# Kernel optimization log

Measured on AMD Instinct MI355X. Metric: run time of the kernel, lower is better.

Reference implementation:

```python
import jax, jax.numpy as jnp
import numpy as np

B, L, D, MAXW = 8, 512, 768, 12
H = D // 2  # forward/backward half of the bidirectional encoder output


def setup_inputs() -> dict:
    key = jax.random.key(0)
    k1, k2, k3, k4 = jax.random.split(key, 4)
    h = jax.random.normal(k1, (B, L, D), jnp.float32)
    # ATG-style span enumeration: start=i, end=min(i+w, L-1) for w in [0, MAXW)
    starts = jnp.broadcast_to(jnp.arange(L)[:, None], (L, MAXW))
    ends = jnp.minimum(starts + jnp.arange(MAXW)[None, :], L - 1)
    span_idx = jnp.stack([starts, ends], axis=-1).reshape(1, L * MAXW, 2)
    span_idx = jnp.broadcast_to(span_idx, (B, L * MAXW, 2)).astype(jnp.int64)
    # downproject: Linear(D -> D) since BidirectionalEndpointSpanExtractor output dim == D
    W = jax.random.normal(k2, (D, D), jnp.float32) / np.sqrt(D)
    b = jnp.zeros((D,), jnp.float32)
    # learned sentinels (use_sentinels=True default), one per half
    start_sentinel = jax.random.normal(k3, (H,), jnp.float32) * 0.02
    end_sentinel = jax.random.normal(k4, (H,), jnp.float32) * 0.02
    return {"h": h, "span_idx": span_idx, "W": W, "b": b,
            "start_sentinel": start_sentinel, "end_sentinel": end_sentinel}


def _gather(seq, idx):
    # seq: (B, L, H), idx: (B, S) -> (B, S, H)
    return jnp.take_along_axis(seq, idx[..., None], axis=1)


def reference(h, span_idx, W, b, start_sentinel, end_sentinel):
    Bv, Lv, Dv = h.shape
    Hv = Dv // 2
    fwd, bwd = h[..., :Hv], h[..., Hv:]
    starts = span_idx[..., 0]
    ends = span_idx[..., 1]
    # exclusive endpoints
    excl_starts = starts - 1
    start_mask = excl_starts == -1                 # before sequence start -> start sentinel
    excl_ends = ends + 1
    end_mask = excl_ends >= Lv                     # past sequence end -> end sentinel
    excl_starts = jnp.where(start_mask, 0, excl_starts)
    excl_ends = jnp.where(end_mask, 0, excl_ends)
    f_start = _gather(fwd, excl_starts)            # (B, S, H)
    f_end = _gather(fwd, ends)
    b_start = _gather(bwd, excl_ends)
    b_end = _gather(bwd, starts)
    f_start = jnp.where(start_mask[..., None], start_sentinel, f_start)
    b_start = jnp.where(end_mask[..., None], end_sentinel, b_start)
    # forward_combination='y-x', backward_combination='x-y'
    span_rep = jnp.concatenate([f_end - f_start, b_start - b_end], axis=-1)  # (B, S, D)
    out = jax.nn.relu(jnp.einsum('bsd,ed->bse', span_rep, W) + b)
    return out.reshape(Bv, Lv, -1, Dv)            # (B, L, MAXW, D)
```

## Files before the change

### kernel.cpp

```cpp
#include <hip/hip_runtime.h>

typedef __attribute__((ext_vector_type(4))) float f32x4;
typedef __attribute__((ext_vector_type(8))) _Float16 f16x8;
typedef __attribute__((ext_vector_type(4))) unsigned short u16x4;

#define NB 8
#define LLEN 512
#define DD 768
#define MW 12
#define HH 384
#define TT (NB * LLEN)
#define SS (LLEN * MW)
#define MM (2 * TT)

#define BT 32
#define BE 192
#define WROWS 48
#define PADW 204

#define PACKH_BLOCKS ((TT * 192) / 256)
#define PACKW_BLOCKS ((DD * 192) / 256)
#define SENT_BLOCKS (DD / 4)
#define PREP_BLOCKS (PACKH_BLOCKS + PACKW_BLOCKS + SENT_BLOCKS)

__device__ __forceinline__ unsigned short f2h(float x) {
  _Float16 h = (_Float16)x;
  return __builtin_bit_cast(unsigned short, h);
}
__device__ __forceinline__ float h2f(unsigned short u) {
  return (float)__builtin_bit_cast(_Float16, u);
}
__device__ __forceinline__ void gload_lds16(const void* g, void* l) {
  __builtin_amdgcn_global_load_lds(
      (const __attribute__((address_space(1))) unsigned int*)g,
      (__attribute__((address_space(3))) unsigned int*)l, 16, 0, 0);
}

__global__ __launch_bounds__(256) void prep_k(const float* __restrict__ h,
                                              const float* __restrict__ W,
                                              const float* __restrict__ ss,
                                              const float* __restrict__ es,
                                              unsigned short* __restrict__ A,
                                              unsigned short* __restrict__ Bu,
                                              unsigned short* __restrict__ Bv,
                                              unsigned short* __restrict__ us,
                                              unsigned short* __restrict__ vs) {
  int bid = blockIdx.x;
  if (bid < PACKH_BLOCKS) {
    int idx = bid * 256 + threadIdx.x;
    int t = idx / 192;
    int k = (idx - t * 192) * 4;
    f32x4 f = *(const f32x4*)(h + (size_t)idx * 4);
    int row = (k < HH) ? t : TT + t;
    int kk = (k < HH) ? k : k - HH;
    u16x4 v;
#pragma unroll
    for (int j = 0; j < 4; ++j) v[j] = f2h(f[j]);
    *(u16x4*)(A + (size_t)row * HH + kk) = v;
  } else if (bid < PACKH_BLOCKS + PACKW_BLOCKS) {
    int idx = (bid - PACKH_BLOCKS) * 256 + threadIdx.x;
    int e = idx / 192;
    int k = (idx - e * 192) * 4;
    f32x4 f = *(const f32x4*)(W + (size_t)idx * 4);
    unsigned short* Bm = (k < HH) ? Bu : Bv;
    int kk = (k < HH) ? k : k - HH;
    u16x4 v;
#pragma unroll
    for (int j = 0; j < 4; ++j) v[j] = f2h(f[j]);
    *(u16x4*)(Bm + (size_t)e * HH + kk) = v;
  } else {
    int e = (bid - PACKH_BLOCKS - PACKW_BLOCKS) * 4 + (threadIdx.x >> 6);
    int lane = threadIdx.x & 63;
    float a = 0.f, b = 0.f;
    const float* w = W + (size_t)e * DD;
    for (int j = lane; j < HH; j += 64) {
      a += ss[j] * w[j];
      b += es[j] * w[HH + j];
    }
#pragma unroll
    for (int off = 32; off > 0; off >>= 1) {
      a += __shfl_down(a, off);
      b += __shfl_down(b, off);
    }
    if (lane == 0) { us[e] = f2h(a); vs[e] = f2h(b); }
  }
}

__global__ __launch_bounds__(256) void fused_k(const unsigned short* __restrict__ A,
                                               const unsigned short* __restrict__ Bu,
                                               const unsigned short* __restrict__ Bv,
                                               const int* __restrict__ span,
                                               const unsigned short* __restrict__ us,
                                               const unsigned short* __restrict__ vs,
                                               const float* __restrict__ bias,
                                               float* __restrict__ out) {
  __shared__ char lds[96 * 64 * 2 + 2 * 192 * 64 * 2];
  __shared__ int2 spans[BT * MW];

  const int bid = blockIdx.x;
  const int g = ((bid >> 5) << 3) | (bid & 7);
  const int ec = (bid >> 3) & 3;
  const int b = g >> 4;
  const int tch = g & 15;
  const int T0 = tch * BT;
  const int E0 = ec * BE;

  const int tid = threadIdx.x;
  const int lane = tid & 63;
  const int w = tid >> 6;
  const int wr = w >> 1, wc = w & 1;
  const int l16 = lane & 15, l4 = lane >> 4;

  {
    const int2* sp = (const int2*)span + (size_t)b * SS + (size_t)T0 * MW;
    for (int s = tid; s < BT * MW; s += 256) spans[s] = sp[s];
  }

  unsigned short* As = (unsigned short*)lds;
  unsigned short* Bf = As + 96 * 64;
  unsigned short* Bb = Bf + 192 * 64;

  f32x4 acc[3][6] = {};

  for (int kc = 0; kc < HH; kc += 64) {
#pragma unroll
    for (int r = 0; r < 3; ++r) {
      int o = (r * 256 + tid) * 16;
      int rr = o >> 7, colb = o & 127;
      int tloc = T0 - 1 + (rr < WROWS ? rr : rr - WROWS);
      tloc = min(max(tloc, 0), LLEN - 1);
      size_t arow = (size_t)(rr < WROWS ? 0 : TT) + (size_t)b * LLEN + tloc;
      gload_lds16((const char*)A + (arow * HH + kc) * 2 + colb, (char*)As + o);
    }
#pragma unroll
    for (int r = 0; r < 6; ++r) {
      int o = (r * 256 + tid) * 16;
      int rr = o >> 7, colb = o & 127;
      gload_lds16((const char*)Bu + ((size_t)(E0 + rr) * HH + kc) * 2 + colb, (char*)Bf + o);
      gload_lds16((const char*)Bv + ((size_t)(E0 + rr) * HH + kc) * 2 + colb, (char*)Bb + o);
    }
    __syncthreads();

    const unsigned short* Am = As + (wr * WROWS) * 64;
    const unsigned short* Bm = (wr == 0) ? Bf : Bb;
    f16x8 af[2][3], bf[2][6];
#pragma unroll
    for (int ks = 0; ks < 2; ++ks)
#pragma unroll
      for (int m = 0; m < 3; ++m)
        af[ks][m] = *(const f16x8*)&Am[(m * 16 + l16) * 64 + ks * 32 + l4 * 8];
#pragma unroll
    for (int ks = 0; ks < 2; ++ks)
#pragma unroll
      for (int n = 0; n < 6; ++n)
        bf[ks][n] = *(const f16x8*)&Bm[(wc * 96 + n * 16 + l16) * 64 + ks * 32 + l4 * 8];

#pragma unroll
    for (int m = 0; m < 3; ++m)
#pragma unroll
      for (int n = 0; n < 6; ++n) {
        acc[m][n] = __builtin_amdgcn_mfma_f32_16x16x32_f16(af[0][m], bf[0][n], acc[m][n], 0, 0, 0);
        acc[m][n] = __builtin_amdgcn_mfma_f32_16x16x32_f16(af[1][m], bf[1][n], acc[m][n], 0, 0, 0);
      }
    __syncthreads();
  }

  unsigned short* Uld = (unsigned short*)lds;
  unsigned short* Vld = Uld + WROWS * PADW;
  {
    unsigned short* Cm = (wr == 0) ? Uld : Vld;
#pragma unroll
    for (int m = 0; m < 3; ++m) {
      int row = m * 16 + l4 * 4;
#pragma unroll
      for (int n = 0; n < 6; ++n) {
        int col = wc * 96 + n * 16 + l16;
#pragma unroll
        for (int r = 0; r < 4; ++r)
          Cm[(row + r) * PADW + col] = f2h(acc[m][n][r]);
      }
    }
  }
  __syncthreads();

  const u16x4* U4 = (const u16x4*)Uld;
  const u16x4* V4 = (const u16x4*)Vld;
  const u16x4* us4 = (const u16x4*)us + (E0 >> 2);
  const u16x4* vs4 = (const u16x4*)vs + (E0 >> 2);
  const f32x4* bias4 = (const f32x4*)bias + (E0 >> 2);
  f32x4* out4 = (f32x4*)out + ((size_t)b * SS + (size_t)T0 * MW) * (DD / 4) + (E0 >> 2);

  int e4 = tid % 48;
  int lw = tid / 48;
#pragma unroll 4
  for (int it = 0; it < (BT * MW * 48) / 256; ++it) {
    const int2 se = spans[lw];
    const int start = se.x, end = se.y;
    u16x4 pe = U4[(end - T0 + 1) * 51 + e4];
    u16x4 pv = (end + 1 >= LLEN) ? vs4[e4] : V4[(end - T0 + 2) * 51 + e4];
    u16x4 mu = (start == 0) ? us4[e4] : U4[(start - T0) * 51 + e4];
    u16x4 mv = V4[(start - T0 + 1) * 51 + e4];
    f32x4 bb = bias4[e4];
    f32x4 r;
#pragma unroll
    for (int j = 0; j < 4; ++j) {
      float x = h2f(pe[j]) + h2f(pv[j]) - h2f(mu[j]) - h2f(mv[j]) + bb[j];
      r[j] = fmaxf(x, 0.f);
    }
    out4[(size_t)lw * (DD / 4) + e4] = r;
    e4 += 16; lw += 5;
    if (e4 >= 48) { e4 -= 48; lw += 1; }
  }
}

__global__ __launch_bounds__(256) void naive_k(const float* __restrict__ h,
                                               const int* __restrict__ span,
                                               const float* __restrict__ W,
                                               const float* __restrict__ bias,
                                               const float* __restrict__ ss,
                                               const float* __restrict__ es,
                                               float* __restrict__ out) {
  int bs = blockIdx.x;
  int b = bs / SS;
  int start = span[(size_t)bs * 2 + 0];
  int end   = span[(size_t)bs * 2 + 1];
  __shared__ float rep[DD];
  const float* hb = h + (size_t)b * LLEN * DD;
  for (int k = threadIdx.x; k < HH; k += blockDim.x) {
    float fs = (start == 0) ? ss[k] : hb[(size_t)(start - 1) * DD + k];
    rep[k] = hb[(size_t)end * DD + k] - fs;
    float bstart = (end + 1 >= LLEN) ? es[k] : hb[(size_t)(end + 1) * DD + HH + k];
    rep[HH + k] = bstart - hb[(size_t)start * DD + HH + k];
  }
  __syncthreads();
  for (int e = threadIdx.x; e < DD; e += blockDim.x) {
    const float* w = W + (size_t)e * DD;
    float acc = bias[e];
    for (int k = 0; k < DD; k += 4) {
      acc += rep[k] * w[k] + rep[k + 1] * w[k + 1] + rep[k + 2] * w[k + 2] + rep[k + 3] * w[k + 3];
    }
    out[(size_t)bs * DD + e] = fmaxf(acc, 0.f);
  }
}

extern "C" void kernel_launch(void* const* d_in, const int* in_sizes, int n_in,
                              void* d_out, int out_size, void* d_ws, size_t ws_size,
                              hipStream_t stream) {
  const float* h  = (const float*)d_in[0];
  const int* span = (const int*)d_in[1];
  const float* W  = (const float*)d_in[2];
  const float* bias = (const float*)d_in[3];
  const float* ss = (const float*)d_in[4];
  const float* es = (const float*)d_in[5];
  float* out = (float*)d_out;

  const size_t szA  = (size_t)MM * HH * sizeof(unsigned short);
  const size_t szB  = (size_t)DD * HH * sizeof(unsigned short);
  const size_t szS  = DD * sizeof(unsigned short);
  const size_t need = szA + 2 * szB + 2 * szS;

  if (ws_size < need) {
    naive_k<<<NB * SS, 256, 0, stream>>>(h, span, W, bias, ss, es, out);
    return;
  }

  char* ws = (char*)d_ws;
  unsigned short* A  = (unsigned short*)ws;
  unsigned short* Bu = A + (size_t)MM * HH;
  unsigned short* Bv = Bu + (size_t)DD * HH;
  unsigned short* us = Bv + (size_t)DD * HH;
  unsigned short* vs = us + DD;

  prep_k<<<PREP_BLOCKS, 256, 0, stream>>>(h, W, ss, es, A, Bu, Bv, us, vs);
  fused_k<<<512, 256, 0, stream>>>(A, Bu, Bv, span, us, vs, bias, out);
}
```

Baseline: 49.73 us.

## Shrink output-column tile to 64, swizzle LDS, and triple grid size

Reduces the per-block output-column tile from 192 to 64, so the grid grows from 512 to 1536 blocks and each block uses far less LDS and fewer accumulator registers. An occupancy hint of 4 blocks per CU is added via launch bounds. An XOR swizzle on the 16-byte LDS slots removes bank conflicts on the fragment reads, and the block-to-tile mapping becomes a plain column-major order. The cost is that A tiles are reloaded three times as often, and the earlier grouped rasterization for L2 reuse is dropped.

New measurement: 50.54 us. About the same (+1.6%).

```diff
diff --git a/kernel.cpp b/kernel.cpp
--- a/kernel.cpp
+++ b/kernel.cpp
@@ -14,9 +14,9 @@
 #define MM (2 * TT)
 
 #define BT 32
-#define BE 192
+#define BE 64
 #define WROWS 48
-#define PADW 204
+#define PUV 68
 
 #define PACKH_BLOCKS ((TT * 192) / 256)
 #define PACKW_BLOCKS ((DD * 192) / 256)
@@ -86,20 +86,20 @@
   }
 }
 
-__global__ __launch_bounds__(256) void fused_k(const unsigned short* __restrict__ A,
-                                               const unsigned short* __restrict__ Bu,
-                                               const unsigned short* __restrict__ Bv,
-                                               const int* __restrict__ span,
-                                               const unsigned short* __restrict__ us,
-                                               const unsigned short* __restrict__ vs,
-                                               const float* __restrict__ bias,
-                                               float* __restrict__ out) {
-  __shared__ char lds[96 * 64 * 2 + 2 * 192 * 64 * 2];
+__global__ __launch_bounds__(256, 4) void fused_k(const unsigned short* __restrict__ A,
+                                                  const unsigned short* __restrict__ Bu,
+                                                  const unsigned short* __restrict__ Bv,
+                                                  const int* __restrict__ span,
+                                                  const unsigned short* __restrict__ us,
+                                                  const unsigned short* __restrict__ vs,
+                                                  const float* __restrict__ bias,
+                                                  float* __restrict__ out) {
+  __shared__ char lds[96 * 128 + 2 * 64 * 128];
   __shared__ int2 spans[BT * MW];
 
   const int bid = blockIdx.x;
-  const int g = ((bid >> 5) << 3) | (bid & 7);
-  const int ec = (bid >> 3) & 3;
+  const int ec = bid >> 7;
+  const int g = bid & 127;
   const int b = g >> 4;
   const int tch = g & 15;
   const int T0 = tch * BT;
@@ -116,49 +116,56 @@
     for (int s = tid; s < BT * MW; s += 256) spans[s] = sp[s];
   }
 
-  unsigned short* As = (unsigned short*)lds;
-  unsigned short* Bf = As + 96 * 64;
-  unsigned short* Bb = Bf + 192 * 64;
-
-  f32x4 acc[3][6] = {};
+  char* As = lds;
+  char* Bf = lds + 96 * 128;
+  char* Bb = Bf + 64 * 128;
+
+  f32x4 acc[3][2] = {};
 
   for (int kc = 0; kc < HH; kc += 64) {
 #pragma unroll
     for (int r = 0; r < 3; ++r) {
       int o = (r * 256 + tid) * 16;
-      int rr = o >> 7, colb = o & 127;
+      int rr = o >> 7;
+      int scol = (((o >> 4) & 7) ^ (rr & 7)) << 4;
       int tloc = T0 - 1 + (rr < WROWS ? rr : rr - WROWS);
       tloc = min(max(tloc, 0), LLEN - 1);
       size_t arow = (size_t)(rr < WROWS ? 0 : TT) + (size_t)b * LLEN + tloc;
-      gload_lds16((const char*)A + (arow * HH + kc) * 2 + colb, (char*)As + o);
-    }
-#pragma unroll
-    for (int r = 0; r < 6; ++r) {
+      gload_lds16((const char*)A + (arow * HH + kc) * 2 + scol, As + o);
+    }
+#pragma unroll
+    for (int r = 0; r < 2; ++r) {
       int o = (r * 256 + tid) * 16;
-      int rr = o >> 7, colb = o & 127;
-      gload_lds16((const char*)Bu + ((size_t)(E0 + rr) * HH + kc) * 2 + colb, (char*)Bf + o);
-      gload_lds16((const char*)Bv + ((size_t)(E0 + rr) * HH + kc) * 2 + colb, (char*)Bb + o);
+      int rr = o >> 7;
+      int scol = (((o >> 4) & 7) ^ (rr & 7)) << 4;
+      gload_lds16((const char*)Bu + ((size_t)(E0 + rr) * HH + kc) * 2 + scol, Bf + o);
+      gload_lds16((const char*)Bv + ((size_t)(E0 + rr) * HH + kc) * 2 + scol, Bb + o);
     }
     __syncthreads();
 
-    const unsigned short* Am = As + (wr * WROWS) * 64;
-    const unsigned short* Bm = (wr == 0) ? Bf : Bb;
-    f16x8 af[2][3], bf[2][6];
+    const char* Bm = (wr == 0) ? Bf : Bb;
+    f16x8 af[2][3], bf[2][2];
 #pragma unroll
     for (int ks = 0; ks < 2; ++ks)
 #pragma unroll
-      for (int m = 0; m < 3; ++m)
-        af[ks][m] = *(const f16x8*)&Am[(m * 16 + l16) * 64 + ks * 32 + l4 * 8];
+      for (int m = 0; m < 3; ++m) {
+        int row = wr * WROWS + m * 16 + l16;
+        int slot = (ks * 4 + l4) ^ (row & 7);
+        af[ks][m] = *(const f16x8*)(As + row * 128 + slot * 16);
+      }
 #pragma unroll
     for (int ks = 0; ks < 2; ++ks)
 #pragma unroll
-      for (int n = 0; n < 6; ++n)
-        bf[ks][n] = *(const f16x8*)&Bm[(wc * 96 + n * 16 + l16) * 64 + ks * 32 + l4 * 8];
+      for (int n = 0; n < 2; ++n) {
+        int row = wc * 32 + n * 16 + l16;
+        int slot = (ks * 4 + l4) ^ (row & 7);
+        bf[ks][n] = *(const f16x8*)(Bm + row * 128 + slot * 16);
+      }
 
 #pragma unroll
     for (int m = 0; m < 3; ++m)
 #pragma unroll
-      for (int n = 0; n < 6; ++n) {
+      for (int n = 0; n < 2; ++n) {
         acc[m][n] = __builtin_amdgcn_mfma_f32_16x16x32_f16(af[0][m], bf[0][n], acc[m][n], 0, 0, 0);
         acc[m][n] = __builtin_amdgcn_mfma_f32_16x16x32_f16(af[1][m], bf[1][n], acc[m][n], 0, 0, 0);
       }
@@ -166,18 +173,18 @@
   }
 
   unsigned short* Uld = (unsigned short*)lds;
-  unsigned short* Vld = Uld + WROWS * PADW;
+  unsigned short* Vld = Uld + WROWS * PUV;
   {
     unsigned short* Cm = (wr == 0) ? Uld : Vld;
 #pragma unroll
     for (int m = 0; m < 3; ++m) {
       int row = m * 16 + l4 * 4;
 #pragma unroll
-      for (int n = 0; n < 6; ++n) {
-        int col = wc * 96 + n * 16 + l16;
+      for (int n = 0; n < 2; ++n) {
+        int col = wc * 32 + n * 16 + l16;
 #pragma unroll
         for (int r = 0; r < 4; ++r)
-          Cm[(row + r) * PADW + col] = f2h(acc[m][n][r]);
+          Cm[(row + r) * PUV + col] = f2h(acc[m][n][r]);
       }
     }
   }
@@ -190,16 +197,16 @@
   const f32x4* bias4 = (const f32x4*)bias + (E0 >> 2);
   f32x4* out4 = (f32x4*)out + ((size_t)b * SS + (size_t)T0 * MW) * (DD / 4) + (E0 >> 2);
 
-  int e4 = tid % 48;
-  int lw = tid / 48;
+  const int e4 = tid & 15;
+  int lw = tid >> 4;
 #pragma unroll 4
-  for (int it = 0; it < (BT * MW * 48) / 256; ++it) {
+  for (int it = 0; it < (BT * MW) / 16; ++it) {
     const int2 se = spans[lw];
     const int start = se.x, end = se.y;
-    u16x4 pe = U4[(end - T0 + 1) * 51 + e4];
-    u16x4 pv = (end + 1 >= LLEN) ? vs4[e4] : V4[(end - T0 + 2) * 51 + e4];
-    u16x4 mu = (start == 0) ? us4[e4] : U4[(start - T0) * 51 + e4];
-    u16x4 mv = V4[(start - T0 + 1) * 51 + e4];
+    u16x4 pe = U4[(end - T0 + 1) * 17 + e4];
+    u16x4 pv = (end + 1 >= LLEN) ? vs4[e4] : V4[(end - T0 + 2) * 17 + e4];
+    u16x4 mu = (start == 0) ? us4[e4] : U4[(start - T0) * 17 + e4];
+    u16x4 mv = V4[(start - T0 + 1) * 17 + e4];
     f32x4 bb = bias4[e4];
     f32x4 r;
 #pragma unroll
@@ -208,8 +215,7 @@
       r[j] = fmaxf(x, 0.f);
     }
     out4[(size_t)lw * (DD / 4) + e4] = r;
-    e4 += 16; lw += 5;
-    if (e4 >= 48) { e4 -= 48; lw += 1; }
+    lw += 16;
   }
 }
 
@@ -272,5 +278,5 @@
   unsigned short* vs = us + DD;
 
   prep_k<<<PREP_BLOCKS, 256, 0, stream>>>(h, W, ss, es, A, Bu, Bv, us, vs);
-  fused_k<<<512, 256, 0, stream>>>(A, Bu, Bv, span, us, vs, bias, out);
-}
+  fused_k<<<12 * 128, 256, 0, stream>>>(A, Bu, Bv, span, us, vs, bias, out);
+}
```
